# Optimization experiments

Hardware: AMD Instinct MI355X
Metric: run time of the kernel (lower is better)

Reference implementation:

```python
import jax, jax.numpy as jnp
import numpy as np

CUTOFF = 5.0        # init kwarg: cutoff
CUTOFF_SHELL = 2.0  # init kwarg: cutoff_shell (skin); nbl built with cutoff+shell
BOX = 20.0          # simulation box extent (no PBC: cell=0, pbc=False)


def setup_inputs() -> dict:
    key = jax.random.key(0)
    # [n_molecules, n_atoms, 3] positions, uniform in a 20 A box
    positions = jax.random.uniform(key, (64, 512, 3), dtype=jnp.float32) * BOX
    return {"positions": positions}


def reference(positions):
    # Batched, vectorized equivalent of the per-molecule Python loop:
    # for each molecule, pairs (i,j), i != j, with |r_i - r_j| < cutoff + shell.
    M, N, _ = positions.shape
    rc = CUTOFF + CUTOFF_SHELL
    # Rij[m,i,j] = r_j - r_i  (displacement vectors, as SchNet nbl transforms emit)
    Rij = positions[:, None, :, :] - positions[:, :, None, :]   # [M,N,N,3]
    d2 = jnp.sum(Rij * Rij, axis=-1)                            # [M,N,N]
    self_mask = jnp.eye(N, dtype=bool)                          # exclude i==j
    nbh_mask = (d2 < rc * rc) & ~self_mask                      # [M,N,N] bool
    # Dense, static-shape representation of the collated ragged neighbor list:
    # masked displacement vectors (zero outside cutoff). idx_i/idx_j with
    # molecule offsets are exactly nonzero(nbh_mask) in a dynamic-shape world.
    return Rij * nbh_mask[..., None].astype(Rij.dtype)
```

## Files before the change

kernel.cpp:

```cpp
#include <hip/hip_runtime.h>


#define NMOL   64
#define NATOM  512
#define RC2    49.0f
#define SLICES 32

typedef unsigned int   u32;
typedef unsigned short u16;
typedef float f32x4 __attribute__((ext_vector_type(4)));

__device__ __forceinline__ float bf2f(u16 u) {
    union { u32 u; float f; } v; v.u = ((u32)u) << 16; return v.f;
}

__global__ __launch_bounds__(256)
void nbl_kernel(const void* __restrict__ pos_raw, float* __restrict__ out) {
    __shared__ float s_row[4][NATOM * 3];
    __shared__ int s_f32;
    const int t = threadIdx.x;

    if (t == 0) s_f32 = 0;
    __syncthreads();
    {
        const u32* w = (const u32*)pos_raw;
        const u32 a = w[t];
        const u32 b = w[t + 256];
        if ((((a >> 8) & 0xffu) > 0x41u) || (((b >> 8) & 0xffu) > 0x41u))
            s_f32 = 1;
    }
    __syncthreads();
    const bool is_f32 = (s_f32 != 0);

    const int bx     = blockIdx.x;
    const int m      = bx >> 5;
    const int slice  = bx & (SLICES - 1);
    const int lane   = t & 63;
    const int wave   = t >> 6;
    const int i_base = slice * 16 + wave * 4;

    const float* pm32 = (const float*)pos_raw + (size_t)m * (NATOM * 3);
    const u16*   pm16 = (const u16*)pos_raw   + (size_t)m * (NATOM * 3);

    float pj[24];
    float ri[12];
    if (is_f32) {
        const float4* p4 = (const float4*)pm32 + lane * 6;
        #pragma unroll
        for (int k = 0; k < 6; ++k) {
            const float4 q = p4[k];
            pj[4*k+0] = q.x; pj[4*k+1] = q.y; pj[4*k+2] = q.z; pj[4*k+3] = q.w;
        }
        #pragma unroll
        for (int r = 0; r < 4; ++r) {
            const int i = i_base + r;
            ri[3*r+0] = pm32[3*i+0];
            ri[3*r+1] = pm32[3*i+1];
            ri[3*r+2] = pm32[3*i+2];
        }
    } else {
        const uint4* p4 = (const uint4*)pm16 + lane * 3;
        u32 words[12];
        #pragma unroll
        for (int k = 0; k < 3; ++k) {
            const uint4 q = p4[k];
            words[4*k+0] = q.x; words[4*k+1] = q.y;
            words[4*k+2] = q.z; words[4*k+3] = q.w;
        }
        #pragma unroll
        for (int k = 0; k < 12; ++k) {
            pj[2*k]   = bf2f((u16)(words[k] & 0xffffu));
            pj[2*k+1] = bf2f((u16)(words[k] >> 16));
        }
        #pragma unroll
        for (int r = 0; r < 4; ++r) {
            const int i = i_base + r;
            ri[3*r+0] = bf2f(pm16[3*i+0]);
            ri[3*r+1] = bf2f(pm16[3*i+1]);
            ri[3*r+2] = bf2f(pm16[3*i+2]);
        }
    }

    const int j0 = lane * 8;
    float* sw = s_row[wave];

    #pragma unroll
    for (int r = 0; r < 4; ++r) {
        const int i = i_base + r;
        const float rix = ri[3*r+0], riy = ri[3*r+1], riz = ri[3*r+2];

        float o[24];
        #pragma unroll
        for (int jj = 0; jj < 8; ++jj) {
            const float dx = __fsub_rn(pj[3*jj+0], rix);
            const float dy = __fsub_rn(pj[3*jj+1], riy);
            const float dz = __fsub_rn(pj[3*jj+2], riz);
            const float d2 = __fadd_rn(__fadd_rn(__fmul_rn(dx, dx),
                                                 __fmul_rn(dy, dy)),
                                       __fmul_rn(dz, dz));
            const bool keep = (d2 < RC2) && ((j0 + jj) != i);
            o[3*jj+0] = keep ? dx : 0.0f;
            o[3*jj+1] = keep ? dy : 0.0f;
            o[3*jj+2] = keep ? dz : 0.0f;
        }

        float4* wp = (float4*)(sw + lane * 24);
        #pragma unroll
        for (int k = 0; k < 6; ++k)
            wp[k] = make_float4(o[4*k+0], o[4*k+1], o[4*k+2], o[4*k+3]);

        const size_t row = (size_t)(m * NATOM + i);
        f32x4* ob = (f32x4*)out + row * 384;
        const f32x4* sr = (const f32x4*)sw;
        #pragma unroll
        for (int k = 0; k < 6; ++k)
            __builtin_nontemporal_store(sr[k * 64 + lane], &ob[k * 64 + lane]);
    }
}

extern "C" void kernel_launch(void* const* d_in, const int* in_sizes, int n_in,
                              void* d_out, int out_size, void* d_ws, size_t ws_size,
                              hipStream_t stream) {
    const void* pos = d_in[0];
    float* out = (float*)d_out;
    dim3 grid(NMOL * SLICES);
    dim3 block(256);
    nbl_kernel<<<grid, block, 0, stream>>>(pos, out);
}
```

Baseline: 202.7 us.

## Store keep-masks in LDS and recompute coalesced outputs from per-lane positions

Instead of staging full 24-float output rows through shared memory, each wave now writes only a per-j keep mask (as 0/1 floats) to LDS. Each lane then recomputes its coalesced float4 output chunk directly from a second, coalesced copy of the positions, multiplying by the mask. The grid is doubled to 64 slices with 2 rows per wave, and nontemporal stores become plain stores. This cuts LDS traffic at the cost of extra position loads, component-select logic and more blocks. Multiplying by the mask instead of selecting turns a non-finite displacement into NaN where the old code wrote zero.

```diff
diff --git a/kernel.cpp b/kernel.cpp
--- a/kernel.cpp
+++ b/kernel.cpp
@@ -4,11 +4,10 @@
 #define NMOL   64
 #define NATOM  512
 #define RC2    49.0f
-#define SLICES 32
+#define SLICES 64
 
 typedef unsigned int   u32;
 typedef unsigned short u16;
-typedef float f32x4 __attribute__((ext_vector_type(4)));
 
 __device__ __forceinline__ float bf2f(u16 u) {
     union { u32 u; float f; } v; v.u = ((u32)u) << 16; return v.f;
@@ -16,7 +15,7 @@
 
 __global__ __launch_bounds__(256)
 void nbl_kernel(const void* __restrict__ pos_raw, float* __restrict__ out) {
-    __shared__ float s_row[4][NATOM * 3];
+    __shared__ float s_keep[4][NATOM];
     __shared__ int s_f32;
     const int t = threadIdx.x;
 
@@ -33,17 +32,18 @@
     const bool is_f32 = (s_f32 != 0);
 
     const int bx     = blockIdx.x;
-    const int m      = bx >> 5;
+    const int m      = bx >> 6;
     const int slice  = bx & (SLICES - 1);
     const int lane   = t & 63;
     const int wave   = t >> 6;
-    const int i_base = slice * 16 + wave * 4;
+    const int i_base = slice * 8 + wave * 2;
 
     const float* pm32 = (const float*)pos_raw + (size_t)m * (NATOM * 3);
     const u16*   pm16 = (const u16*)pos_raw   + (size_t)m * (NATOM * 3);
 
     float pj[24];
-    float ri[12];
+    float pc[24];
+    float ri[6];
     if (is_f32) {
         const float4* p4 = (const float4*)pm32 + lane * 6;
         #pragma unroll
@@ -51,12 +51,16 @@
             const float4 q = p4[k];
             pj[4*k+0] = q.x; pj[4*k+1] = q.y; pj[4*k+2] = q.z; pj[4*k+3] = q.w;
         }
+        const float4* c4 = (const float4*)pm32;
         #pragma unroll
-        for (int r = 0; r < 4; ++r) {
+        for (int k = 0; k < 6; ++k) {
+            const float4 q = c4[64*k + lane];
+            pc[4*k+0] = q.x; pc[4*k+1] = q.y; pc[4*k+2] = q.z; pc[4*k+3] = q.w;
+        }
+        #pragma unroll
+        for (int r = 0; r < 2; ++r) {
             const int i = i_base + r;
-            ri[3*r+0] = pm32[3*i+0];
-            ri[3*r+1] = pm32[3*i+1];
-            ri[3*r+2] = pm32[3*i+2];
+            ri[3*r+0] = pm32[3*i+0]; ri[3*r+1] = pm32[3*i+1]; ri[3*r+2] = pm32[3*i+2];
         }
     } else {
         const uint4* p4 = (const uint4*)pm16 + lane * 3;
@@ -72,8 +76,17 @@
             pj[2*k]   = bf2f((u16)(words[k] & 0xffffu));
             pj[2*k+1] = bf2f((u16)(words[k] >> 16));
         }
+        const uint2* c2 = (const uint2*)pm16;
         #pragma unroll
-        for (int r = 0; r < 4; ++r) {
+        for (int k = 0; k < 6; ++k) {
+            const uint2 q = c2[64*k + lane];
+            pc[4*k+0] = bf2f((u16)(q.x & 0xffffu));
+            pc[4*k+1] = bf2f((u16)(q.x >> 16));
+            pc[4*k+2] = bf2f((u16)(q.y & 0xffffu));
+            pc[4*k+3] = bf2f((u16)(q.y >> 16));
+        }
+        #pragma unroll
+        for (int r = 0; r < 2; ++r) {
             const int i = i_base + r;
             ri[3*r+0] = bf2f(pm16[3*i+0]);
             ri[3*r+1] = bf2f(pm16[3*i+1]);
@@ -81,40 +94,59 @@
         }
     }
 
+    int cms[6], jas[6];
+    #pragma unroll
+    for (int k = 0; k < 6; ++k) {
+        const int c = 64 * k + lane;
+        cms[k] = c % 3;
+        jas[k] = (4 * c) / 3;
+    }
+
     const int j0 = lane * 8;
-    float* sw = s_row[wave];
+    float* kw = s_keep[wave];
 
     #pragma unroll
-    for (int r = 0; r < 4; ++r) {
+    for (int r = 0; r < 2; ++r) {
         const int i = i_base + r;
-        const float rix = ri[3*r+0], riy = ri[3*r+1], riz = ri[3*r+2];
+        const float rx = ri[3*r+0], ry = ri[3*r+1], rz = ri[3*r+2];
 
-        float o[24];
+        float kv[8];
         #pragma unroll
         for (int jj = 0; jj < 8; ++jj) {
-            const float dx = __fsub_rn(pj[3*jj+0], rix);
-            const float dy = __fsub_rn(pj[3*jj+1], riy);
-            const float dz = __fsub_rn(pj[3*jj+2], riz);
+            const float dx = __fsub_rn(pj[3*jj+0], rx);
+            const float dy = __fsub_rn(pj[3*jj+1], ry);
+            const float dz = __fsub_rn(pj[3*jj+2], rz);
             const float d2 = __fadd_rn(__fadd_rn(__fmul_rn(dx, dx),
                                                  __fmul_rn(dy, dy)),
                                        __fmul_rn(dz, dz));
-            const bool keep = (d2 < RC2) && ((j0 + jj) != i);
-            o[3*jj+0] = keep ? dx : 0.0f;
-            o[3*jj+1] = keep ? dy : 0.0f;
-            o[3*jj+2] = keep ? dz : 0.0f;
+            kv[jj] = ((d2 < RC2) && ((j0 + jj) != i)) ? 1.0f : 0.0f;
         }
-
-        float4* wp = (float4*)(sw + lane * 24);
-        #pragma unroll
-        for (int k = 0; k < 6; ++k)
-            wp[k] = make_float4(o[4*k+0], o[4*k+1], o[4*k+2], o[4*k+3]);
+        float4* kw4 = (float4*)(kw + j0);
+        kw4[0] = make_float4(kv[0], kv[1], kv[2], kv[3]);
+        kw4[1] = make_float4(kv[4], kv[5], kv[6], kv[7]);
 
         const size_t row = (size_t)(m * NATOM + i);
-        f32x4* ob = (f32x4*)out + row * 384;
-        const f32x4* sr = (const f32x4*)sw;
+        float4* ob = (float4*)out + row * 384;
         #pragma unroll
-        for (int k = 0; k < 6; ++k)
-            __builtin_nontemporal_store(sr[k * 64 + lane], &ob[k * 64 + lane]);
+        for (int k = 0; k < 6; ++k) {
+            const int cm = cms[k];
+            const int ja = jas[k];
+            const float ka = kw[ja];
+            const float kb = kw[ja + 1];
+            const float r0 = (cm == 0) ? rx : ((cm == 1) ? ry : rz);
+            const float r1 = (cm == 0) ? ry : ((cm == 1) ? rz : rx);
+            const float r2 = (cm == 0) ? rz : ((cm == 1) ? rx : ry);
+            const float m0 = ka;
+            const float m1 = (cm == 2) ? kb : ka;
+            const float m2 = (cm == 0) ? ka : kb;
+            const float m3 = kb;
+            float4 o;
+            o.x = __fmul_rn(__fsub_rn(pc[4*k+0], r0), m0);
+            o.y = __fmul_rn(__fsub_rn(pc[4*k+1], r1), m1);
+            o.z = __fmul_rn(__fsub_rn(pc[4*k+2], r2), m2);
+            o.w = __fmul_rn(__fsub_rn(pc[4*k+3], r0), m3);
+            ob[64 * k + lane] = o;
+        }
     }
 }
 
```

New measurement: 193.1 us (median of 2 runs). 1.05x faster.
